# Performance work log

Measured on AMD Instinct MI355X. Metric: run time of the kernel, lower is better.

## Reference

```python
import jax, jax.numpy as jnp
import numpy as np

N_ROIS = 2000
FH, FW, C = 50, 50, 512
PH, PW = 7, 7
N_CLASS = 21
IMG = 800
FC_IN = PH * PW * C  # 25088
FC_OUT = 4096


def crop_and_resize(img, boxes, ph, pw):
    """Faithful jax port of tf.image.crop_and_resize (bilinear, extrapolation 0).
    img: [H, W, C]; boxes: [N, 4] normalized (y1, x1, y2, x2). Returns [N, ph, pw, C]."""
    H, W, _ = img.shape
    y1, x1, y2, x2 = boxes[:, 0], boxes[:, 1], boxes[:, 2], boxes[:, 3]
    iy = jnp.arange(ph, dtype=boxes.dtype)
    ix = jnp.arange(pw, dtype=boxes.dtype)
    # TF sampling grid: in_y = y1*(H-1) + i * (y2-y1)*(H-1)/(crop_h-1)
    in_y = y1[:, None] * (H - 1) + iy[None, :] * ((y2 - y1)[:, None] * (H - 1) / (ph - 1))  # [N, ph]
    in_x = x1[:, None] * (W - 1) + ix[None, :] * ((x2 - x1)[:, None] * (W - 1) / (pw - 1))  # [N, pw]
    y0f = jnp.floor(in_y); x0f = jnp.floor(in_x)
    ylerp = (in_y - y0f)[:, :, None, None]   # [N, ph, 1, 1]
    xlerp = (in_x - x0f)[:, None, :, None]   # [N, 1, pw, 1]
    y0 = jnp.clip(y0f, 0, H - 1).astype(jnp.int32)
    y1i = jnp.clip(y0f + 1, 0, H - 1).astype(jnp.int32)
    x0 = jnp.clip(x0f, 0, W - 1).astype(jnp.int32)
    x1i = jnp.clip(x0f + 1, 0, W - 1).astype(jnp.int32)

    def gather(yi, xi):  # [N,ph],[N,pw] -> [N,ph,pw,C]
        return img[yi[:, :, None], xi[:, None, :]]

    top = gather(y0, x0) * (1 - xlerp) + gather(y0, x1i) * xlerp
    bot = gather(y1i, x0) * (1 - xlerp) + gather(y1i, x1i) * xlerp
    out = top * (1 - ylerp) + bot * ylerp
    valid = ((in_y >= 0) & (in_y <= H - 1))[:, :, None] & ((in_x >= 0) & (in_x <= W - 1))[:, None, :]
    return jnp.where(valid[..., None], out, jnp.zeros((), out.dtype))


def setup_inputs() -> dict:
    key = jax.random.key(0)
    kf, ky, kx, k1, k2, k3, k4, k5, k6 = jax.random.split(key, 9)
    feature = jax.random.normal(kf, (1, FH, FW, C), dtype=jnp.float32)
    # valid boxes in original-image coordinates: y1<y2, x1<x2 within [0, IMG]
    ys = jnp.sort(jax.random.uniform(ky, (N_ROIS, 2), dtype=jnp.float32) * IMG, axis=1)
    xs = jnp.sort(jax.random.uniform(kx, (N_ROIS, 2), dtype=jnp.float32) * IMG, axis=1)
    rois = jnp.stack([ys[:, 0], xs[:, 0], ys[:, 1], xs[:, 1]], axis=1)
    W_fc = jax.random.normal(k1, (FC_IN, FC_OUT), dtype=jnp.float32) * 0.01
    b_fc = jnp.zeros((FC_OUT,), dtype=jnp.float32)
    W_loc = jax.random.normal(k3, (FC_OUT, N_CLASS * 4), dtype=jnp.float32) * 0.01
    b_loc = jnp.zeros((N_CLASS * 4,), dtype=jnp.float32)
    W_score = jax.random.normal(k5, (FC_OUT, N_CLASS), dtype=jnp.float32) * 0.01
    b_score = jnp.zeros((N_CLASS,), dtype=jnp.float32)
    return {"feature": feature, "rois": rois, "img_h": IMG, "img_w": IMG,
            "W_fc": W_fc, "b_fc": b_fc, "W_loc": W_loc, "b_loc": b_loc,
            "W_score": W_score, "b_score": b_score}


def reference(feature, rois, img_h, img_w, W_fc, b_fc, W_loc, b_loc, W_score, b_score):
    norm = jnp.array([img_h, img_w, img_h, img_w], dtype=jnp.float32)
    boxes = rois / norm                      # normalized [y1,x1,y2,x2]
    pool = crop_and_resize(feature[0], boxes, PH, PW)  # [N, 7, 7, 512]
    flat = pool.reshape(rois.shape[0], -1)   # [N, 25088]
    fc = flat @ W_fc + b_fc                  # [N, 4096]
    roi_cls_locs = fc @ W_loc + b_loc        # [N, 84]
    roi_scores = fc @ W_score + b_score      # [N, 21]
    return roi_cls_locs, roi_scores
```

## Files before the change

### kernel.cpp

```cpp
#include <hip/hip_runtime.h>
#include <stdint.h>


typedef float          f32x4 __attribute__((ext_vector_type(4)));
typedef __bf16         bfx8  __attribute__((ext_vector_type(8)));
typedef unsigned short u16x8 __attribute__((ext_vector_type(8)));

#define KBIG 25088
#define NMID 4096
#define NROIS 2000
#define G1BLOCKS 784
#define SPLITS 28

__device__ __forceinline__ unsigned short f2bf(float f) {
  unsigned int u = __float_as_uint(f);
  return (unsigned short)((u + 0x7fffu + ((u >> 16) & 1u)) >> 16);
}

__device__ __forceinline__ void gll16(const void* g, void* l) {
  __builtin_amdgcn_global_load_lds(
      (const __attribute__((address_space(1))) void*)(uintptr_t)(g),
      (__attribute__((address_space(3))) void*)(uintptr_t)(l), 16, 0, 0);
}

__global__ __launch_bounds__(256) void k_prep(const float* __restrict__ Wl,
                                              const float* __restrict__ Ws,
                                              const float* __restrict__ bfc,
                                              const float* __restrict__ bl,
                                              const float* __restrict__ bs,
                                              unsigned short* __restrict__ WcatT,
                                              float* __restrict__ bc) {
  if (blockIdx.x < 2048) {
    int idx = blockIdx.x * 256 + threadIdx.x;
    int c = idx >> 12, k = idx & 4095;
    float v = 0.0f;
    if (c < 84)       v = Wl[k * 84 + c];
    else if (c < 105) v = Ws[k * 21 + (c - 84)];
    WcatT[idx] = f2bf(v);
  } else {
    int c = blockIdx.x - 2048;
    int t = threadIdx.x;
    __shared__ float red[256];
    float p = 0.0f;
    if (c < 105) {
      for (int k = t; k < 4096; k += 256) {
        float w = (c < 84) ? Wl[k * 84 + c] : Ws[k * 21 + (c - 84)];
        p += bfc[k] * w;
      }
    }
    red[t] = p;
    __syncthreads();
    for (int s = 128; s > 0; s >>= 1) {
      if (t < s) red[t] += red[t + s];
      __syncthreads();
    }
    if (t == 0) {
      float bias = (c < 84) ? bl[c] : (c < 105 ? bs[c - 84] : 0.0f);
      bc[c] = (c < 105) ? (red[0] + bias) : 0.0f;
    }
  }
}

__global__ __launch_bounds__(256, 3) void k_pool_gemm1(
    const float* __restrict__ F, const float* __restrict__ rois,
    const int* __restrict__ ihp, const int* __restrict__ iwp,
    unsigned short* __restrict__ A,
    const float* __restrict__ Wfc, const unsigned short* __restrict__ WcatT,
    float* __restrict__ Pg1) {
  const int t = threadIdx.x;
  __shared__ __align__(16) char sB[32768];
  if (blockIdx.x < G1BLOCKS) {
    const int lane = t & 63, wid = t >> 6;
    const int l15 = lane & 15, l4 = lane >> 4;
    const int mt = blockIdx.x >> 1, sp = blockIdx.x & 1;
    const int m0 = mt * 64;
    const int kbase = sp * 2048;
    const int jlog = (t & 7) ^ ((t >> 3) & 7);
    f32x4 acc[8] = {};
    f32x4 rA[4], rB[4];

    const float* aptr = Wfc + (size_t)(m0 + wid * 16 + l15) * NMID + kbase + l4 * 8;

    auto stageB = [&](int c, int off) {
#pragma unroll
      for (int q = 0; q < 4; ++q)
        gll16(WcatT + (size_t)(q * 32 + (t >> 3)) * NMID + kbase + c * 64 + jlog * 8,
              sB + off + q * 4096 + wid * 1024);
    };
    auto loadA = [&](f32x4* dst, int c) {
      dst[0] = *(const f32x4*)(aptr + c * 64);
      dst[1] = *(const f32x4*)(aptr + c * 64 + 4);
      dst[2] = *(const f32x4*)(aptr + c * 64 + 32);
      dst[3] = *(const f32x4*)(aptr + c * 64 + 36);
    };
    auto cvtA = [&](bfx8& af0, bfx8& af1, const f32x4* r) {
      u16x8 p0, p1;
#pragma unroll
      for (int i = 0; i < 4; ++i) {
        p0[i] = f2bf(r[0][i]); p0[i + 4] = f2bf(r[1][i]);
        p1[i] = f2bf(r[2][i]); p1[i + 4] = f2bf(r[3][i]);
      }
      af0 = *(bfx8*)&p0; af1 = *(bfx8*)&p1;
    };
    auto compute = [&](int off, bfx8 af0, bfx8 af1) {
#pragma unroll
      for (int kk = 0; kk < 2; ++kk) {
        bfx8 bfr[8];
#pragma unroll
        for (int nt = 0; nt < 8; ++nt) {
          const int row = nt * 16 + l15;
          bfr[nt] = *(const bfx8*)(sB + off + row * 128 + ((((kk << 2) + l4) ^ (row & 7)) << 4));
        }
        const bfx8 af = kk ? af1 : af0;
#pragma unroll
        for (int nt = 0; nt < 8; ++nt)
          acc[nt] = __builtin_amdgcn_mfma_f32_16x16x32_bf16(af, bfr[nt], acc[nt], 0, 0, 0);
      }
    };

    stageB(0, 0);
    __builtin_amdgcn_sched_barrier(0);
    loadA(rA, 0);
    loadA(rB, 1);
    for (int cc = 0; cc < 16; ++cc) {
      const int c0 = cc * 2;
      bfx8 af0, af1;
      cvtA(af0, af1, rA);
      stageB(c0 + 1, 16384);
      __builtin_amdgcn_sched_barrier(0);
      loadA(rA, (c0 + 2 < 32) ? c0 + 2 : 31);
      asm volatile("s_waitcnt vmcnt(12)" ::: "memory");
      __builtin_amdgcn_s_barrier();
      __builtin_amdgcn_sched_barrier(0);
      compute(0, af0, af1);
      __builtin_amdgcn_s_barrier();
      cvtA(af0, af1, rB);
      stageB((c0 + 2 < 32) ? c0 + 2 : 31, 0);
      __builtin_amdgcn_sched_barrier(0);
      loadA(rB, (c0 + 3 < 32) ? c0 + 3 : 31);
      asm volatile("s_waitcnt vmcnt(12)" ::: "memory");
      __builtin_amdgcn_s_barrier();
      __builtin_amdgcn_sched_barrier(0);
      compute(16384, af0, af1);
      __builtin_amdgcn_s_barrier();
    }
    asm volatile("s_waitcnt vmcnt(0)" ::: "memory");
#pragma unroll
    for (int nt = 0; nt < 8; ++nt) {
      const int n = nt * 16 + l15;
      float* dst = Pg1 + ((size_t)sp * 128 + n) * KBIG + m0 + wid * 16 + l4 * 4;
      *(f32x4*)dst = acc[nt];
    }
  } else {
    const int r = blockIdx.x - G1BLOCKS;
    const float ih = (float)ihp[0], iw = (float)iwp[0];
    const float y1 = rois[r * 4 + 0] / ih;
    const float x1 = rois[r * 4 + 1] / iw;
    const float y2 = rois[r * 4 + 2] / ih;
    const float x2 = rois[r * 4 + 3] / iw;
    const float sy = (y2 - y1) * 49.0f / 6.0f;
    const float sx = (x2 - x1) * 49.0f / 6.0f;
    const int ch = t * 2;
    unsigned int* __restrict__ Arow = (unsigned int*)(A + (size_t)r * KBIG);
    for (int cell = 0; cell < 49; ++cell) {
      const int iy = cell / 7, ix = cell - iy * 7;
      const float in_y = y1 * 49.0f + (float)iy * sy;
      const float in_x = x1 * 49.0f + (float)ix * sx;
      const float y0f = floorf(in_y), x0f = floorf(in_x);
      const float yl = in_y - y0f, xl = in_x - x0f;
      const int y0  = (int)fminf(fmaxf(y0f, 0.0f), 49.0f);
      const int y1i = (int)fminf(fmaxf(y0f + 1.0f, 0.0f), 49.0f);
      const int x0  = (int)fminf(fmaxf(x0f, 0.0f), 49.0f);
      const int x1i = (int)fminf(fmaxf(x0f + 1.0f, 0.0f), 49.0f);
      const bool valid = (in_y >= 0.0f) && (in_y <= 49.0f) &&
                         (in_x >= 0.0f) && (in_x <= 49.0f);
      float2 f00 = *(const float2*)&F[(y0 * 50 + x0) * 512 + ch];
      float2 f01 = *(const float2*)&F[(y0 * 50 + x1i) * 512 + ch];
      float2 f10 = *(const float2*)&F[(y1i * 50 + x0) * 512 + ch];
      float2 f11 = *(const float2*)&F[(y1i * 50 + x1i) * 512 + ch];
      float o0 = 0.0f, o1 = 0.0f;
      if (valid) {
        float t0 = f00.x * (1.0f - xl) + f01.x * xl;
        float t1 = f00.y * (1.0f - xl) + f01.y * xl;
        float b0 = f10.x * (1.0f - xl) + f11.x * xl;
        float b1 = f10.y * (1.0f - xl) + f11.y * xl;
        o0 = t0 * (1.0f - yl) + b0 * yl;
        o1 = t1 * (1.0f - yl) + b1 * yl;
      }
      Arow[(cell * 512 + ch) >> 1] =
          (unsigned int)f2bf(o0) | ((unsigned int)f2bf(o1) << 16);
    }
  }
}

__global__ __launch_bounds__(256) void k_addcvt(const float* __restrict__ Pg1,
                                                unsigned short* __restrict__ WcT) {
  const size_t i = ((size_t)blockIdx.x * 256 + threadIdx.x) * 8;
  f32x4 a0 = *(const f32x4*)(Pg1 + i);
  f32x4 a1 = *(const f32x4*)(Pg1 + i + 4);
  f32x4 b0 = *(const f32x4*)(Pg1 + 3211264 + i);
  f32x4 b1 = *(const f32x4*)(Pg1 + 3211264 + i + 4);
  u16x8 o;
#pragma unroll
  for (int j = 0; j < 4; ++j) {
    o[j]     = f2bf(a0[j] + b0[j]);
    o[j + 4] = f2bf(a1[j] + b1[j]);
  }
  *(u16x8*)(WcT + i) = o;
}

__global__ __launch_bounds__(256) void k_gemm2(const unsigned short* __restrict__ Ap,
                                               const unsigned short* __restrict__ WcT,
                                               float* __restrict__ P) {
  __shared__ __align__(16) char S[49152];
  const int t = threadIdx.x;
  const int lane = t & 63, wid = t >> 6;
  const int wm = wid >> 1, wn = wid & 1;
  const int l15 = lane & 15, l4 = lane >> 4;
  const int mt = blockIdx.x, sp = blockIdx.y;
  const int kbase = sp * 896;
  const int jlog = (t & 7) ^ ((t >> 3) & 7);
  f32x4 acc[2][4] = {};

  int ar0 = mt * 64 + (t >> 3);
  int ar1 = ar0 + 32;
  if (ar0 > NROIS - 1) ar0 = NROIS - 1;
  if (ar1 > NROIS - 1) ar1 = NROIS - 1;
  const unsigned short* asrc0 = Ap + (size_t)ar0 * KBIG + jlog * 8;
  const unsigned short* asrc1 = Ap + (size_t)ar1 * KBIG + jlog * 8;

  auto stage2 = [&](int c, int off) {
    const int k0 = kbase + c * 64;
    gll16(asrc0 + k0, S + off + wid * 1024);
    gll16(asrc1 + k0, S + off + 4096 + wid * 1024);
#pragma unroll
    for (int q = 0; q < 4; ++q)
      gll16(WcT + (size_t)(q * 32 + (t >> 3)) * KBIG + k0 + jlog * 8,
            S + off + 8192 + q * 4096 + wid * 1024);
  };
  auto compute2 = [&](int off) {
#pragma unroll
    for (int kh = 0; kh < 2; ++kh) {
      bfx8 af[2], bfr[4];
#pragma unroll
      for (int mi = 0; mi < 2; ++mi) {
        const int row = wm * 32 + mi * 16 + l15;
        af[mi] = *(const bfx8*)(S + off + row * 128 + ((((kh << 2) + l4) ^ (row & 7)) << 4));
      }
#pragma unroll
      for (int ni = 0; ni < 4; ++ni) {
        const int row = wn * 64 + ni * 16 + l15;
        bfr[ni] = *(const bfx8*)(S + off + 8192 + row * 128 + ((((kh << 2) + l4) ^ (row & 7)) << 4));
      }
#pragma unroll
      for (int mi = 0; mi < 2; ++mi)
#pragma unroll
        for (int ni = 0; ni < 4; ++ni)
          acc[mi][ni] = __builtin_amdgcn_mfma_f32_16x16x32_bf16(af[mi], bfr[ni], acc[mi][ni], 0, 0, 0);
    }
  };

  stage2(0, 0);
  for (int cc = 0; cc < 7; ++cc) {
    const int c0 = cc * 2;
    stage2(c0 + 1, 24576);
    asm volatile("s_waitcnt vmcnt(6)" ::: "memory");
    __builtin_amdgcn_s_barrier();
    __builtin_amdgcn_sched_barrier(0);
    compute2(0);
    __builtin_amdgcn_s_barrier();
    stage2((c0 + 2 < 14) ? c0 + 2 : 13, 0);
    asm volatile("s_waitcnt vmcnt(6)" ::: "memory");
    __builtin_amdgcn_s_barrier();
    __builtin_amdgcn_sched_barrier(0);
    compute2(24576);
    __builtin_amdgcn_s_barrier();
  }
  asm volatile("s_waitcnt vmcnt(0)" ::: "memory");
  float* out = P + (size_t)(mt * SPLITS + sp) * 8192;
#pragma unroll
  for (int mi = 0; mi < 2; ++mi)
#pragma unroll
    for (int ni = 0; ni < 4; ++ni)
#pragma unroll
      for (int i = 0; i < 4; ++i)
        out[(wm * 32 + mi * 16 + l4 * 4 + i) * 128 + wn * 64 + ni * 16 + l15] = acc[mi][ni][i];
}

__global__ __launch_bounds__(128) void k_reduce(const float* __restrict__ P,
                                                const float* __restrict__ bc,
                                                float* __restrict__ out) {
  const int m = blockIdx.x;
  const int c = threadIdx.x;
  if (c >= 105) return;
  const int mt = m >> 6, r = m & 63;
  float sum = 0.0f;
#pragma unroll
  for (int s = 0; s < SPLITS; ++s)
    sum += P[(size_t)(mt * SPLITS + s) * 8192 + r * 128 + c];
  sum += bc[c];
  if (c < 84) out[m * 84 + c] = sum;
  else        out[168000 + m * 21 + (c - 84)] = sum;
}

extern "C" void kernel_launch(void* const* d_in, const int* in_sizes, int n_in,
                              void* d_out, int out_size, void* d_ws, size_t ws_size,
                              hipStream_t stream) {
  const float* F    = (const float*)d_in[0];
  const float* rois = (const float*)d_in[1];
  const int*   ih   = (const int*)d_in[2];
  const int*   iw   = (const int*)d_in[3];
  const float* Wfc  = (const float*)d_in[4];
  const float* bfc  = (const float*)d_in[5];
  const float* Wl   = (const float*)d_in[6];
  const float* bl   = (const float*)d_in[7];
  const float* Ws   = (const float*)d_in[8];
  const float* bs   = (const float*)d_in[9];
  (void)in_sizes; (void)n_in; (void)out_size; (void)ws_size;

  char* ws = (char*)d_ws;
  unsigned short* Apool = (unsigned short*)(ws);
  unsigned short* WcatT = (unsigned short*)(ws + 100352000);
  unsigned short* WcT   = (unsigned short*)(ws + 101400576);
  float*          bc    = (float*)(ws + 107823104);
  float*          P     = (float*)(ws + 107823616);
  float*          Pg1   = (float*)(ws + 137183744);
  float*          out   = (float*)d_out;

  k_prep      <<<2176, 256, 0, stream>>>(Wl, Ws, bfc, bl, bs, WcatT, bc);
  k_pool_gemm1<<<G1BLOCKS + NROIS, 256, 0, stream>>>(F, rois, ih, iw, Apool,
                                                     Wfc, WcatT, Pg1);
  k_addcvt    <<<1568, 256, 0, stream>>>(Pg1, WcT);
  k_gemm2     <<<dim3(32, SPLITS), 256, 0, stream>>>(Apool, WcT, P);
  k_reduce    <<<NROIS, 128, 0, stream>>>(P, bc, out);
}
```

Measured before the change: 232.9 us.

## Stage W_fc tiles through LDS with coalesced loads and prefetch pool gathers

The fused pool/GEMM1 kernel now loads W_fc tiles with coalesced row-wise float4 reads, converts them to bf16 and writes them to a double-buffered swizzled LDS tile. MFMA A fragments are then read from LDS. Before, each lane did strided per-row loads straight into registers. The pooling blocks also software-pipeline the bilinear gathers, fetching the next cell's four feature samples while the current cell is interpolated. The cost is 16 KB more shared memory per block, which may lower occupancy at launch bounds of 3, plus extra LDS writes and changed wait counts.

```diff
diff --git a/kernel.cpp b/kernel.cpp
--- a/kernel.cpp
+++ b/kernel.cpp
@@ -5,6 +5,7 @@
 typedef float          f32x4 __attribute__((ext_vector_type(4)));
 typedef __bf16         bfx8  __attribute__((ext_vector_type(8)));
 typedef unsigned short u16x8 __attribute__((ext_vector_type(8)));
+typedef unsigned short u16x4 __attribute__((ext_vector_type(4)));
 
 #define KBIG 25088
 #define NMID 4096
@@ -68,6 +69,7 @@
     const float* __restrict__ Wfc, const unsigned short* __restrict__ WcatT,
     float* __restrict__ Pg1) {
   const int t = threadIdx.x;
+  __shared__ __align__(16) char sA[16384];
   __shared__ __align__(16) char sB[32768];
   if (blockIdx.x < G1BLOCKS) {
     const int lane = t & 63, wid = t >> 6;
@@ -77,74 +79,83 @@
     const int kbase = sp * 2048;
     const int jlog = (t & 7) ^ ((t >> 3) & 7);
     f32x4 acc[8] = {};
-    f32x4 rA[4], rB[4];
-
-    const float* aptr = Wfc + (size_t)(m0 + wid * 16 + l15) * NMID + kbase + l4 * 8;
-
+    f32x4 rE[4], rO[4];
+
+    const float* abase = Wfc + (size_t)m0 * NMID + kbase;
+    const int arw = t >> 4;
+    const int acl = (t & 15) * 4;
+    const int ac16 = (t & 15) >> 1;
+    const int ahalf = t & 1;
+
+    auto loadA = [&](f32x4* d, int c) {
+#pragma unroll
+      for (int i = 0; i < 4; ++i)
+        d[i] = *(const f32x4*)(abase + (size_t)(i * 16 + arw) * NMID + c * 64 + acl);
+    };
+    auto putA = [&](const f32x4* r, int off) {
+#pragma unroll
+      for (int i = 0; i < 4; ++i) {
+        const int row = i * 16 + arw;
+        u16x4 p;
+#pragma unroll
+        for (int j = 0; j < 4; ++j) p[j] = f2bf(r[i][j]);
+        *(u16x4*)(sA + off + row * 128 + ((ac16 ^ (row & 7)) << 4) + ahalf * 8) = p;
+      }
+    };
     auto stageB = [&](int c, int off) {
 #pragma unroll
       for (int q = 0; q < 4; ++q)
         gll16(WcatT + (size_t)(q * 32 + (t >> 3)) * NMID + kbase + c * 64 + jlog * 8,
               sB + off + q * 4096 + wid * 1024);
     };
-    auto loadA = [&](f32x4* dst, int c) {
-      dst[0] = *(const f32x4*)(aptr + c * 64);
-      dst[1] = *(const f32x4*)(aptr + c * 64 + 4);
-      dst[2] = *(const f32x4*)(aptr + c * 64 + 32);
-      dst[3] = *(const f32x4*)(aptr + c * 64 + 36);
-    };
-    auto cvtA = [&](bfx8& af0, bfx8& af1, const f32x4* r) {
-      u16x8 p0, p1;
-#pragma unroll
-      for (int i = 0; i < 4; ++i) {
-        p0[i] = f2bf(r[0][i]); p0[i + 4] = f2bf(r[1][i]);
-        p1[i] = f2bf(r[2][i]); p1[i + 4] = f2bf(r[3][i]);
-      }
-      af0 = *(bfx8*)&p0; af1 = *(bfx8*)&p1;
-    };
-    auto compute = [&](int off, bfx8 af0, bfx8 af1) {
+    auto compute = [&](int aoff, int boff) {
 #pragma unroll
       for (int kk = 0; kk < 2; ++kk) {
+        const int ar = wid * 16 + l15;
+        bfx8 af = *(const bfx8*)(sA + aoff + ar * 128 + ((((kk << 2) + l4) ^ (ar & 7)) << 4));
         bfx8 bfr[8];
 #pragma unroll
         for (int nt = 0; nt < 8; ++nt) {
           const int row = nt * 16 + l15;
-          bfr[nt] = *(const bfx8*)(sB + off + row * 128 + ((((kk << 2) + l4) ^ (row & 7)) << 4));
+          bfr[nt] = *(const bfx8*)(sB + boff + row * 128 + ((((kk << 2) + l4) ^ (row & 7)) << 4));
         }
-        const bfx8 af = kk ? af1 : af0;
 #pragma unroll
         for (int nt = 0; nt < 8; ++nt)
           acc[nt] = __builtin_amdgcn_mfma_f32_16x16x32_bf16(af, bfr[nt], acc[nt], 0, 0, 0);
       }
     };
 
+    loadA(rE, 0);
+    __builtin_amdgcn_sched_barrier(0);
     stageB(0, 0);
     __builtin_amdgcn_sched_barrier(0);
-    loadA(rA, 0);
-    loadA(rB, 1);
+    loadA(rO, 1);
+    __builtin_amdgcn_sched_barrier(0);
+    putA(rE, 0);
+
     for (int cc = 0; cc < 16; ++cc) {
       const int c0 = cc * 2;
-      bfx8 af0, af1;
-      cvtA(af0, af1, rA);
-      stageB(c0 + 1, 16384);
-      __builtin_amdgcn_sched_barrier(0);
-      loadA(rA, (c0 + 2 < 32) ? c0 + 2 : 31);
-      asm volatile("s_waitcnt vmcnt(12)" ::: "memory");
+      putA(rO, 8192);
+      stageB((c0 + 1 < 32) ? c0 + 1 : 31, 16384);
+      __builtin_amdgcn_sched_barrier(0);
+      loadA(rE, (c0 + 2 < 32) ? c0 + 2 : 31);
+      __builtin_amdgcn_sched_barrier(0);
+      asm volatile("s_waitcnt vmcnt(8) lgkmcnt(0)" ::: "memory");
       __builtin_amdgcn_s_barrier();
       __builtin_amdgcn_sched_barrier(0);
-      compute(0, af0, af1);
+      compute(0, 0);
       __builtin_amdgcn_s_barrier();
-      cvtA(af0, af1, rB);
+      putA(rE, 0);
       stageB((c0 + 2 < 32) ? c0 + 2 : 31, 0);
       __builtin_amdgcn_sched_barrier(0);
-      loadA(rB, (c0 + 3 < 32) ? c0 + 3 : 31);
-      asm volatile("s_waitcnt vmcnt(12)" ::: "memory");
+      loadA(rO, (c0 + 3 < 32) ? c0 + 3 : 31);
+      __builtin_amdgcn_sched_barrier(0);
+      asm volatile("s_waitcnt vmcnt(8) lgkmcnt(0)" ::: "memory");
       __builtin_amdgcn_s_barrier();
       __builtin_amdgcn_sched_barrier(0);
-      compute(16384, af0, af1);
+      compute(8192, 16384);
       __builtin_amdgcn_s_barrier();
     }
-    asm volatile("s_waitcnt vmcnt(0)" ::: "memory");
 #pragma unroll
     for (int nt = 0; nt < 8; ++nt) {
       const int n = nt * 16 + l15;
@@ -162,33 +173,52 @@
     const float sx = (x2 - x1) * 49.0f / 6.0f;
     const int ch = t * 2;
     unsigned int* __restrict__ Arow = (unsigned int*)(A + (size_t)r * KBIG);
-    for (int cell = 0; cell < 49; ++cell) {
+
+    auto cellcoords = [&](int cell, int& o00, int& o01, int& o10, int& o11,
+                          float& yl, float& xl, bool& valid) {
       const int iy = cell / 7, ix = cell - iy * 7;
       const float in_y = y1 * 49.0f + (float)iy * sy;
       const float in_x = x1 * 49.0f + (float)ix * sx;
       const float y0f = floorf(in_y), x0f = floorf(in_x);
-      const float yl = in_y - y0f, xl = in_x - x0f;
+      yl = in_y - y0f; xl = in_x - x0f;
       const int y0  = (int)fminf(fmaxf(y0f, 0.0f), 49.0f);
       const int y1i = (int)fminf(fmaxf(y0f + 1.0f, 0.0f), 49.0f);
       const int x0  = (int)fminf(fmaxf(x0f, 0.0f), 49.0f);
       const int x1i = (int)fminf(fmaxf(x0f + 1.0f, 0.0f), 49.0f);
-      const bool valid = (in_y >= 0.0f) && (in_y <= 49.0f) &&
-                         (in_x >= 0.0f) && (in_x <= 49.0f);
-      float2 f00 = *(const float2*)&F[(y0 * 50 + x0) * 512 + ch];
-      float2 f01 = *(const float2*)&F[(y0 * 50 + x1i) * 512 + ch];
-      float2 f10 = *(const float2*)&F[(y1i * 50 + x0) * 512 + ch];
-      float2 f11 = *(const float2*)&F[(y1i * 50 + x1i) * 512 + ch];
-      float o0 = 0.0f, o1 = 0.0f;
-      if (valid) {
-        float t0 = f00.x * (1.0f - xl) + f01.x * xl;
-        float t1 = f00.y * (1.0f - xl) + f01.y * xl;
-        float b0 = f10.x * (1.0f - xl) + f11.x * xl;
-        float b1 = f10.y * (1.0f - xl) + f11.y * xl;
-        o0 = t0 * (1.0f - yl) + b0 * yl;
-        o1 = t1 * (1.0f - yl) + b1 * yl;
+      valid = (in_y >= 0.0f) && (in_y <= 49.0f) && (in_x >= 0.0f) && (in_x <= 49.0f);
+      o00 = (y0 * 50 + x0) * 512;  o01 = (y0 * 50 + x1i) * 512;
+      o10 = (y1i * 50 + x0) * 512; o11 = (y1i * 50 + x1i) * 512;
+    };
+
+    int o00, o01, o10, o11; float yl, xl; bool valid;
+    cellcoords(0, o00, o01, o10, o11, yl, xl, valid);
+    float2 f00 = *(const float2*)&F[o00 + ch];
+    float2 f01 = *(const float2*)&F[o01 + ch];
+    float2 f10 = *(const float2*)&F[o10 + ch];
+    float2 f11 = *(const float2*)&F[o11 + ch];
+
+    for (int cell = 0; cell < 49; ++cell) {
+      const float2 g00 = f00, g01 = f01, g10 = f10, g11 = f11;
+      const float pyl = yl, pxl = xl;
+      const bool pv = valid;
+      if (cell < 48) {
+        cellcoords(cell + 1, o00, o01, o10, o11, yl, xl, valid);
+        f00 = *(const float2*)&F[o00 + ch];
+        f01 = *(const float2*)&F[o01 + ch];
+        f10 = *(const float2*)&F[o10 + ch];
+        f11 = *(const float2*)&F[o11 + ch];
+      }
+      float oA = 0.0f, oB = 0.0f;
+      if (pv) {
+        float t0 = g00.x * (1.0f - pxl) + g01.x * pxl;
+        float t1 = g00.y * (1.0f - pxl) + g01.y * pxl;
+        float b0 = g10.x * (1.0f - pxl) + g11.x * pxl;
+        float b1 = g10.y * (1.0f - pxl) + g11.y * pxl;
+        oA = t0 * (1.0f - pyl) + b0 * pyl;
+        oB = t1 * (1.0f - pyl) + b1 * pyl;
       }
       Arow[(cell * 512 + ch) >> 1] =
-          (unsigned int)f2bf(o0) | ((unsigned int)f2bf(o1) << 16);
+          (unsigned int)f2bf(oA) | ((unsigned int)f2bf(oB) << 16);
     }
   }
 }
```

After: 220.5 us. 1.06x faster.
